# Optimization experiments

Hardware: AMD Instinct MI355X
Metric: run time of the kernel (lower is better)

Reference implementation:

```python
import jax, jax.numpy as jnp
import numpy as np

B, N, KD, VD, ID, H = 2, 2048, 1024, 1024, 1024, 16
HD = ID // H
SCALE = ID ** (-0.5)  # module quirk: scale uses inner_dim, not head_dim
EPS = 1e-5


def layernorm(x, g, b):
    mu = jnp.mean(x, axis=-1, keepdims=True)
    var = jnp.var(x, axis=-1, keepdims=True)
    return (x - mu) * jax.lax.rsqrt(var + EPS) * g + b


def setup_inputs() -> dict:
    key = jax.random.key(0)
    ks = jax.random.split(key, 12)
    d = {
        "keys": jax.random.normal(ks[0], (B, N, KD), jnp.float32),
        "values": jax.random.normal(ks[1], (B, N, VD), jnp.float32),
        "qk_norm_g": jnp.ones((KD,), jnp.float32),
        "qk_norm_b": jnp.zeros((KD,), jnp.float32),
        "value_norm_g": jnp.ones((VD,), jnp.float32),
        "value_norm_b": jnp.zeros((VD,), jnp.float32),
        "key_norm_g": jnp.ones((ID,), jnp.float32),
        "key_norm_b": jnp.zeros((ID,), jnp.float32),
        "query_norm_g": jnp.ones((ID,), jnp.float32),
        "query_norm_b": jnp.zeros((ID,), jnp.float32),
        "w_qk": jax.random.normal(ks[2], (KD, 2 * ID), jnp.float32) * (KD ** -0.5),
        "w_v": jax.random.normal(ks[3], (VD, ID), jnp.float32) * (VD ** -0.5),
        "w_out": jax.random.normal(ks[4], (ID, VD), jnp.float32) * (ID ** -0.5),
        "b_out": jnp.zeros((VD,), jnp.float32),
    }
    return d


def reference(keys, values, qk_norm_g, qk_norm_b, value_norm_g, value_norm_b,
              key_norm_g, key_norm_b, query_norm_g, query_norm_b,
              w_qk, w_v, w_out, b_out):
    keys = layernorm(keys, qk_norm_g, qk_norm_b)
    values = layernorm(values, value_norm_g, value_norm_b)
    qk = keys @ w_qk  # [B,N,2*ID]
    q, k = qk[..., :ID], qk[..., ID:]
    q = layernorm(q, query_norm_g, query_norm_b)
    k = layernorm(k, key_norm_g, key_norm_b)
    # b n (h d) -> b h n d
    q = q.reshape(B, N, H, HD).transpose(0, 2, 1, 3)
    k = k.reshape(B, N, H, HD).transpose(0, 2, 1, 3)
    v = (values @ w_v).reshape(B, N, H, HD).transpose(0, 2, 1, 3)
    dots = jnp.einsum('bhqd,bhkd->bhqk', q, k) * SCALE
    attn = jax.nn.softmax(dots, axis=-1)
    out = jnp.einsum('bhqk,bhkd->bhqd', attn, v)
    out = out.transpose(0, 2, 1, 3).reshape(B, N, ID)
    return out @ w_out + b_out
```

## Files before the change

### kernel.cpp

```cpp
#include <hip/hip_runtime.h>
#include <hip/hip_bf16.h>
#include <type_traits>


typedef __hip_bfloat16 bf16;
typedef __attribute__((ext_vector_type(8))) short bf16x8;
typedef __attribute__((ext_vector_type(4))) float f32x4;

#define MFMA_BF16(a, b, c) __builtin_amdgcn_mfma_f32_16x16x32_bf16((a), (b), (c), 0, 0, 0)

__device__ __forceinline__ float us2f(unsigned short u) {
  unsigned int v = ((unsigned int)u) << 16;
  return __builtin_bit_cast(float, v);
}

__device__ __forceinline__ unsigned pack_bf16x2(float a, float b) {
  union { __hip_bfloat162 h; unsigned u; } cv;
  cv.h = __float22bfloat162_rn(float2{a, b});
  return cv.u;
}

__device__ __forceinline__ unsigned pack_bf16x2_trunc(float a, float b) {
  return __builtin_amdgcn_perm(__builtin_bit_cast(unsigned, b),
                               __builtin_bit_cast(unsigned, a), 0x07060302u);
}

__device__ __forceinline__ void gl_lds16(const bf16* g, bf16* l) {
  __builtin_amdgcn_global_load_lds(
      (const __attribute__((address_space(1))) void*)g,
      (__attribute__((address_space(3))) void*)l, 16, 0, 0);
}

__device__ __forceinline__ void barrier_pinned() {
  __builtin_amdgcn_s_barrier();
  __builtin_amdgcn_sched_barrier(0);
}

template <typename TIN>
__device__ __forceinline__ void ln_core(
    const TIN* __restrict__ in, const float* __restrict__ gamma,
    const float* __restrict__ beta, bf16* __restrict__ out,
    int stride, int D, float sc, int row, float* red)
{
  const int t = threadIdx.x;
  float x0, x1, x2, x3;
  if constexpr (std::is_same_v<TIN, float>) {
    float4 u = *(const float4*)(in + (size_t)row * stride + t * 4);
    x0 = u.x; x1 = u.y; x2 = u.z; x3 = u.w;
  } else {
    ushort4 u = *(const ushort4*)(in + (size_t)row * stride + t * 4);
    x0 = us2f(u.x); x1 = us2f(u.y); x2 = us2f(u.z); x3 = us2f(u.w);
  }
  float s = x0 + x1 + x2 + x3;
  float s2 = x0 * x0 + x1 * x1 + x2 * x2 + x3 * x3;
#pragma unroll
  for (int m = 1; m < 64; m <<= 1) {
    s += __shfl_xor(s, m);
    s2 += __shfl_xor(s2, m);
  }
  const int w = t >> 6, lane = t & 63;
  if (lane == 0) { red[w] = s; red[4 + w] = s2; }
  __syncthreads();
  if (t == 0) {
    float S = red[0] + red[1] + red[2] + red[3];
    float S2 = red[4] + red[5] + red[6] + red[7];
    float mu = S / (float)D;
    float var = S2 / (float)D - mu * mu;
    red[8] = mu;
    red[9] = rsqrtf(var + 1e-5f);
  }
  __syncthreads();
  const float mu = red[8], rs = red[9];
  float4 g4 = *(const float4*)(gamma + t * 4);
  float4 b4 = *(const float4*)(beta + t * 4);
  uint2 o;
  o.x = pack_bf16x2(((x0 - mu) * rs * g4.x + b4.x) * sc, ((x1 - mu) * rs * g4.y + b4.y) * sc);
  o.y = pack_bf16x2(((x2 - mu) * rs * g4.z + b4.z) * sc, ((x3 - mu) * rs * g4.w + b4.w) * sc);
  *(uint2*)(out + (size_t)row * D + t * 4) = o;
}

template <typename TIN>
__global__ __launch_bounds__(256) void ln2_kernel(
    const TIN* __restrict__ in0, const TIN* __restrict__ in1, int stride,
    const float* __restrict__ g0, const float* __restrict__ b0,
    const float* __restrict__ g1, const float* __restrict__ b1,
    bf16* __restrict__ out0, bf16* __restrict__ out1, int D,
    float sc0, float sc1)
{
  __shared__ float red[10];
  const int which = blockIdx.y;
  ln_core<TIN>(which ? in1 : in0, which ? g1 : g0, which ? b1 : b0,
               which ? out1 : out0, stride, D, which ? sc1 : sc0,
               blockIdx.x, red);
}

__device__ __forceinline__ void transpose_core(
    const float* __restrict__ in, bf16* __restrict__ out, int C,
    int r0, int c0, float (*tile)[68])
{
  const int R = 1024;
  const int t = threadIdx.x;
  const int lr = t >> 2, lc = (t & 3) * 16;
  const float* src = in + (size_t)(r0 + lr) * C + (c0 + lc);
#pragma unroll
  for (int i = 0; i < 4; ++i) {
    float4 u = *(const float4*)(src + i * 4);
    tile[lr][lc + i * 4 + 0] = u.x;
    tile[lr][lc + i * 4 + 1] = u.y;
    tile[lr][lc + i * 4 + 2] = u.z;
    tile[lr][lc + i * 4 + 3] = u.w;
  }
  __syncthreads();
  __align__(16) bf16 tmp[16];
#pragma unroll
  for (int j = 0; j < 16; ++j) tmp[j] = __float2bfloat16(tile[lc + j][lr]);
  bf16* dst = out + (size_t)(c0 + lr) * R + (r0 + lc);
  *(bf16x8*)dst       = *(const bf16x8*)&tmp[0];
  *(bf16x8*)(dst + 8) = *(const bf16x8*)&tmp[8];
}

__global__ __launch_bounds__(256) void prep_kernel(
    const float* __restrict__ keys, const float* __restrict__ values,
    const float* __restrict__ qk_g, const float* __restrict__ qk_b,
    const float* __restrict__ val_g, const float* __restrict__ val_b,
    bf16* __restrict__ keys_ln, bf16* __restrict__ values_ln,
    const float* __restrict__ w_qk, bf16* __restrict__ wqkT,
    const float* __restrict__ w_v, bf16* __restrict__ wvT,
    const float* __restrict__ w_out, bf16* __restrict__ woutT)
{
  __shared__ float tile[64][68];
  __shared__ float red[10];
  const int bid = blockIdx.x;
  if (bid < 8192) {
    const int row = bid >> 1, which = bid & 1;
    ln_core<float>(which ? values : keys, which ? val_g : qk_g,
                   which ? val_b : qk_b, which ? values_ln : keys_ln,
                   1024, 1024, 1.0f, row, red);
  } else {
    const int tz = bid - 8192;
    if (tz < 512) {
      transpose_core(w_qk, wqkT, 2048, (tz >> 5) * 64, (tz & 31) * 64, tile);
    } else if (tz < 768) {
      const int s = tz - 512;
      transpose_core(w_v, wvT, 1024, (s >> 4) * 64, (s & 15) * 64, tile);
    } else {
      const int s = tz - 768;
      transpose_core(w_out, woutT, 1024, (s >> 4) * 64, (s & 15) * 64, tile);
    }
  }
}

template <int BM, int BN, int TMODE, typename TOUT>
__device__ __forceinline__ void gemm_core(
    const bf16* __restrict__ A, const bf16* __restrict__ Bt,
    const float* __restrict__ bias, TOUT* __restrict__ C,
    int N, int K, int has_bias, int bx, int by, bf16* smem)
{
  constexpr int MT = BM / 32, NT = BN / 32;
  constexpr int ASL = BM / 32, BSL = BN / 32;
  constexpr int BUFE = (BM + BN) * 64;
  const int t = threadIdx.x;
  const int w = t >> 6, lane = t & 63, l15 = lane & 15, quad = lane >> 4;
  const int wy = w >> 1, wx = w & 1;
  const bf16* Ab = A + (size_t)by * BM * K;
  const bf16* Bb = Bt + (size_t)bx * BN * K;
  f32x4 acc[MT][NT] = {};

  const bf16* aptr[ASL];
  const bf16* bptr[BSL];
#pragma unroll
  for (int i = 0; i < ASL; ++i) {
    int s = i * 256 + t, row = s >> 3, c = (s & 7) ^ (row & 7);
    aptr[i] = Ab + (size_t)row * K + (c << 3);
  }
#pragma unroll
  for (int i = 0; i < BSL; ++i) {
    int s = i * 256 + t, row = s >> 3, c = (s & 7) ^ (row & 7);
    bptr[i] = Bb + (size_t)row * K + (c << 3);
  }

  auto stage = [&](bf16* buf, int kc) {
#pragma unroll
    for (int i = 0; i < ASL; ++i)
      gl_lds16(aptr[i] + kc, buf + (i * 256 + t) * 8);
#pragma unroll
    for (int i = 0; i < BSL; ++i)
      gl_lds16(bptr[i] + kc, buf + BM * 64 + (i * 256 + t) * 8);
  };

  const int sw = (quad ^ (l15 & 7)) << 3;
  const int NK = K >> 6;

  stage(smem, 0);

  for (int kt = 0; kt < NK; ++kt) {
    const int cur = kt & 1;
    bf16* lA = smem + cur * BUFE;
    bf16* lB = lA + BM * 64;
    barrier_pinned();
    if (kt + 1 < NK) {
      stage(smem + (cur ^ 1) * BUFE, (kt + 1) << 6);
      if constexpr (ASL + BSL == 8)
        asm volatile("s_waitcnt vmcnt(8)" ::: "memory");
      else
        asm volatile("s_waitcnt vmcnt(6)" ::: "memory");
    } else {
      asm volatile("s_waitcnt vmcnt(0)" ::: "memory");
    }
    barrier_pinned();

#pragma unroll
    for (int h = 0; h < 2; ++h) {
      const int so = sw ^ (h << 5);
      bf16x8 af[MT], bfr[NT];
#pragma unroll
      for (int mt = 0; mt < MT; ++mt)
        af[mt] = *(const bf16x8*)&lA[(wy * (BM / 2) + mt * 16 + l15) * 64 + so];
#pragma unroll
      for (int nt = 0; nt < NT; ++nt)
        bfr[nt] = *(const bf16x8*)&lB[(wx * (BN / 2) + nt * 16 + l15) * 64 + so];
#pragma unroll
      for (int mt = 0; mt < MT; ++mt)
#pragma unroll
        for (int nt = 0; nt < NT; ++nt)
          acc[mt][nt] = MFMA_BF16(af[mt], bfr[nt], acc[mt][nt]);
    }
  }

  if constexpr (TMODE == 1) {
    constexpr int STR = BM + 8;
    static_assert(BN * STR <= 2 * BUFE, "lOut must fit staging buffers");
    bf16* lOut = smem;
    __syncthreads();
#pragma unroll
    for (int mt = 0; mt < MT; ++mt)
#pragma unroll
      for (int nt = 0; nt < NT; ++nt) {
        const int d = wx * (BN / 2) + nt * 16 + l15;
        const int n = wy * (BM / 2) + mt * 16 + quad * 4;
        uint2 pk;
        pk.x = pack_bf16x2(acc[mt][nt][0], acc[mt][nt][1]);
        pk.y = pack_bf16x2(acc[mt][nt][2], acc[mt][nt][3]);
        *(uint2*)&lOut[d * STR + n] = pk;
      }
    __syncthreads();
    const int row0 = by * BM;
    const int bidx = row0 >> 11, n0 = row0 & 2047;
    const int col0 = bx * BN;
    constexpr int CPR = BM / 32;
    constexpr int NITER = (BN * CPR) / 256;
#pragma unroll
    for (int it = 0; it < NITER; ++it) {
      const int idx = it * 256 + t;
      const int d = idx / CPR, off = (idx % CPR) * 32;
      const bf16* srcp = &lOut[d * STR + off];
      bf16* g = (bf16*)C + ((size_t)(bidx << 10) + col0 + d) * 2048 + n0 + off;
#pragma unroll
      for (int j = 0; j < 4; ++j)
        *(bf16x8*)(g + j * 8) = *(const bf16x8*)(srcp + j * 8);
    }
  } else {
    const int row_base = by * BM + wy * (BM / 2);
    const int col_base = bx * BN + wx * (BN / 2);
#pragma unroll
    for (int mt = 0; mt < MT; ++mt)
#pragma unroll
      for (int nt = 0; nt < NT; ++nt) {
        const int col = col_base + nt * 16 + l15;
        const float bb = has_bias ? bias[col] : 0.0f;
#pragma unroll
        for (int r = 0; r < 4; ++r) {
          const int row = row_base + mt * 16 + quad * 4 + r;
          float v = acc[mt][nt][r] + bb;
          if constexpr (std::is_same_v<TOUT, bf16>)
            C[(size_t)row * N + col] = __float2bfloat16(v);
          else
            C[(size_t)row * N + col] = v;
        }
      }
  }
}

template <int BM, int BN, int TMODE, typename TOUT>
__global__ __launch_bounds__(256) void gemm_bt_kernel(
    const bf16* __restrict__ A, const bf16* __restrict__ Bt,
    const float* __restrict__ bias, TOUT* __restrict__ C,
    int N, int K, int has_bias)
{
  __shared__ __align__(16) bf16 smem[2 * (BM + BN) * 64];
  gemm_core<BM, BN, TMODE, TOUT>(A, Bt, bias, C, N, K, has_bias,
                                 blockIdx.x, blockIdx.y, smem);
}

__global__ __launch_bounds__(256) void gemm_dual_kernel(
    const bf16* __restrict__ A0, const bf16* __restrict__ B0, bf16* __restrict__ C0,
    const bf16* __restrict__ A1, const bf16* __restrict__ B1, bf16* __restrict__ C1)
{
  __shared__ __align__(16) bf16 smem[2 * 256 * 64];
  const int bid = blockIdx.x;
  if (bid < 512) {
    gemm_core<128, 128, 0, bf16>(A0, B0, nullptr, C0, 2048, 1024, 0,
                                 bid & 15, bid >> 4, smem);
  } else {
    const int b = bid - 512;
    gemm_core<128, 128, 1, bf16>(A1, B1, nullptr, C1, 1024, 1024, 0,
                                 b & 7, b >> 3, smem);
  }
}

__global__ __launch_bounds__(256) void flash_kernel(
    const bf16* __restrict__ Q, const bf16* __restrict__ Km,
    const bf16* __restrict__ Vt, bf16* __restrict__ O)
{
  __shared__ __align__(16) bf16 smem[8192 + 8192 + 8192];
  bf16* lQ = smem;
  bf16* lKb = smem + 8192;
  bf16* lVb = smem + 16384;
  const int t = threadIdx.x;
  const int w = t >> 6, lane = t & 63, l15 = lane & 15, quad = lane >> 4;
  const int qt = blockIdx.x, bh = blockIdx.y;
  const int b = bh >> 4, h = bh & 15;
  const int qrow0 = b * 2048 + qt * 128;
  const bf16* qbase = Q + (size_t)qrow0 * 1024 + h * 64;
  const bf16* kbase = Km + ((size_t)(b * 2048)) * 1024 + h * 64;
  const bf16* vbase = Vt + ((size_t)(b * 1024 + h * 64)) * 2048;

  const int sr0 = t >> 3, sc0 = ((t & 7) ^ (sr0 & 7)) << 3;
  const int sr1 = (256 + t) >> 3, sc1 = (((256 + t) & 7) ^ (sr1 & 7)) << 3;
  const int gr0 = (sr0 & 0x23) | ((sr0 & 0x0C) << 1) | ((sr0 & 0x10) >> 2);
  const int gr1 = (sr1 & 0x23) | ((sr1 & 0x0C) << 1) | ((sr1 & 0x10) >> 2);
  const bf16* kp0 = kbase + gr0 * 1024 + sc0;
  const bf16* kp1 = kbase + gr1 * 1024 + sc1;
  const bf16* vp0 = vbase + sr0 * 2048 + sc0;
  const bf16* vp1 = vbase + sr1 * 2048 + sc1;

#pragma unroll
  for (int i = 0; i < 4; ++i) {
    int s = i * 256 + t;
    int row = s >> 3, c = (s & 7) ^ (row & 7);
    gl_lds16(qbase + (size_t)row * 1024 + (c << 3), lQ + s * 8);
  }
  gl_lds16(kp0, lKb + t * 8);
  gl_lds16(kp1, lKb + (256 + t) * 8);
  gl_lds16(vp0, lVb + t * 8);
  gl_lds16(vp1, lVb + (256 + t) * 8);
  asm volatile("s_waitcnt vmcnt(4)" ::: "memory");
  barrier_pinned();

  const int sw = (quad ^ (l15 & 7)) << 3;
  bf16x8 qf[2][2];
#pragma unroll
  for (int mset = 0; mset < 2; ++mset) {
    const int row = w * 32 + mset * 16 + l15;
    qf[mset][0] = *(const bf16x8*)&lQ[row * 64 + sw];
    qf[mset][1] = *(const bf16x8*)&lQ[row * 64 + (sw ^ 32)];
  }

  f32x4 o_acc[4][2] = {};
  f32x4 l_vec[2] = {};

  for (int kt = 0; kt < 32; ++kt) {
    const int cur = kt & 1;
    bf16* lK = lKb + cur * 4096;
    bf16* lV = lVb + cur * 4096;
    bf16* lKn = lKb + (cur ^ 1) * 4096;
    bf16* lVn = lVb + (cur ^ 1) * 4096;

    barrier_pinned();
    {
      const int ktn = (kt + 1) & 31;
      const int ko = ktn << 16;
      const int vo = ktn << 6;
      gl_lds16(kp0 + ko, lKn + t * 8);
      gl_lds16(kp1 + ko, lKn + (256 + t) * 8);
      gl_lds16(vp0 + vo, lVn + t * 8);
      gl_lds16(vp1 + vo, lVn + (256 + t) * 8);
    }
    asm volatile("s_waitcnt vmcnt(4)" ::: "memory");
    barrier_pinned();

    bf16x8 kf[4][2];
#pragma unroll
    for (int nt = 0; nt < 4; ++nt) {
      kf[nt][0] = *(const bf16x8*)&lK[(nt * 16 + l15) * 64 + sw];
      kf[nt][1] = *(const bf16x8*)&lK[(nt * 16 + l15) * 64 + (sw ^ 32)];
    }

    bf16x8 pa[2][2];
#pragma unroll
    for (int mset = 0; mset < 2; ++mset) {
#pragma unroll
      for (int half = 0; half < 2; ++half) {
        f32x4 z0 = {}, z1 = {};
        z0 = MFMA_BF16(kf[2 * half + 0][0], qf[mset][0], z0);
        z0 = MFMA_BF16(kf[2 * half + 0][1], qf[mset][1], z0);
        z1 = MFMA_BF16(kf[2 * half + 1][0], qf[mset][0], z1);
        z1 = MFMA_BF16(kf[2 * half + 1][1], qf[mset][1], z1);
        f32x4 p0, p1;
#pragma unroll
        for (int r = 0; r < 4; ++r) {
          p0[r] = __builtin_amdgcn_exp2f(z0[r]);
          p1[r] = __builtin_amdgcn_exp2f(z1[r]);
        }
        l_vec[mset] += p0 + p1;
        union { unsigned u[4]; bf16x8 v; } cv;
        cv.u[0] = pack_bf16x2_trunc(p0[0], p0[1]);
        cv.u[1] = pack_bf16x2_trunc(p0[2], p0[3]);
        cv.u[2] = pack_bf16x2_trunc(p1[0], p1[1]);
        cv.u[3] = pack_bf16x2_trunc(p1[2], p1[3]);
        pa[mset][half] = cv.v;
      }
    }

    bf16x8 vf[4][2];
#pragma unroll
    for (int dt = 0; dt < 4; ++dt) {
      vf[dt][0] = *(const bf16x8*)&lV[(dt * 16 + l15) * 64 + sw];
      vf[dt][1] = *(const bf16x8*)&lV[(dt * 16 + l15) * 64 + (sw ^ 32)];
    }

    __builtin_amdgcn_s_setprio(1);
#pragma unroll
    for (int mset = 0; mset < 2; ++mset)
#pragma unroll
      for (int dt = 0; dt < 4; ++dt) {
        o_acc[dt][mset] = MFMA_BF16(vf[dt][0], pa[mset][0], o_acc[dt][mset]);
        o_acc[dt][mset] = MFMA_BF16(vf[dt][1], pa[mset][1], o_acc[dt][mset]);
      }
    __builtin_amdgcn_s_setprio(0);
  }

#pragma unroll
  for (int mset = 0; mset < 2; ++mset) {
    float tsum = l_vec[mset][0] + l_vec[mset][1] + l_vec[mset][2] + l_vec[mset][3];
    tsum += __shfl_xor(tsum, 16);
    tsum += __shfl_xor(tsum, 32);
    const float inv = 1.0f / tsum;
    const int m = qrow0 + w * 32 + mset * 16 + l15;
#pragma unroll
    for (int dt = 0; dt < 4; ++dt) {
      uint2 ok;
      ok.x = pack_bf16x2(o_acc[dt][mset][0] * inv, o_acc[dt][mset][1] * inv);
      ok.y = pack_bf16x2(o_acc[dt][mset][2] * inv, o_acc[dt][mset][3] * inv);
      *(uint2*)&O[(size_t)m * 1024 + h * 64 + dt * 16 + quad * 4] = ok;
    }
  }
}

extern "C" void kernel_launch(void* const* d_in, const int* in_sizes, int n_in,
                              void* d_out, int out_size, void* d_ws, size_t ws_size,
                              hipStream_t stream)
{
  (void)in_sizes; (void)n_in; (void)out_size; (void)ws_size;
  const float* keys   = (const float*)d_in[0];
  const float* values = (const float*)d_in[1];
  const float* qk_g   = (const float*)d_in[2];
  const float* qk_b   = (const float*)d_in[3];
  const float* val_g  = (const float*)d_in[4];
  const float* val_b  = (const float*)d_in[5];
  const float* key_g  = (const float*)d_in[6];
  const float* key_b  = (const float*)d_in[7];
  const float* qry_g  = (const float*)d_in[8];
  const float* qry_b  = (const float*)d_in[9];
  const float* w_qk   = (const float*)d_in[10];
  const float* w_v    = (const float*)d_in[11];
  const float* w_out  = (const float*)d_in[12];
  const float* b_out  = (const float*)d_in[13];
  float* out = (float*)d_out;

  const float CEXP = 0.03125f * 1.44269504f;

  char* ws = (char*)d_ws;
  const size_t MB = 1024 * 1024;
  bf16* keys_ln   = (bf16*)(ws + 0);
  bf16* values_ln = (bf16*)(ws + 8 * MB);
  bf16* qk        = (bf16*)(ws + 16 * MB);
  bf16* vt        = (bf16*)(ws + 32 * MB);
  bf16* qln       = (bf16*)(ws + 0);
  bf16* kln       = (bf16*)(ws + 8 * MB);
  bf16* attn      = (bf16*)(ws + 16 * MB);
  bf16* wqkT      = (bf16*)(ws + 40 * MB);
  bf16* wvT       = (bf16*)(ws + 44 * MB);
  bf16* woutT     = (bf16*)(ws + 46 * MB);

  prep_kernel<<<dim3(9216), 256, 0, stream>>>(
      keys, values, qk_g, qk_b, val_g, val_b, keys_ln, values_ln,
      w_qk, wqkT, w_v, wvT, w_out, woutT);
  gemm_dual_kernel<<<dim3(768), 256, 0, stream>>>(
      keys_ln, wqkT, qk, values_ln, wvT, vt);
  ln2_kernel<bf16><<<dim3(4096, 2), 256, 0, stream>>>(
      qk, qk + 1024, 2048, qry_g, qry_b, key_g, key_b, qln, kln, 1024, CEXP, 1.0f);
  flash_kernel<<<dim3(16, 32), 256, 0, stream>>>(qln, kln, vt, attn);
  gemm_bt_kernel<128, 64, 0, float><<<dim3(16, 32), 256, 0, stream>>>(attn, woutT, b_out, out, 1024, 1024, 1);
}
```

Measured before the change: 219.5 us.

## Halve GEMM and flash tile sizes, add XCD-aware block swizzle, MFMA row sums

```diff
diff --git a/kernel.cpp b/kernel.cpp
--- a/kernel.cpp
+++ b/kernel.cpp
@@ -34,6 +34,10 @@
 __device__ __forceinline__ void barrier_pinned() {
   __builtin_amdgcn_s_barrier();
   __builtin_amdgcn_sched_barrier(0);
+}
+
+__device__ __forceinline__ int xcd_swz(int orig, int nwg) {
+  return (orig & 7) * (nwg >> 3) + (orig >> 3);
 }
 
 template <typename TIN>
@@ -288,23 +292,27 @@
     int N, int K, int has_bias)
 {
   __shared__ __align__(16) bf16 smem[2 * (BM + BN) * 64];
+  const int nwg = gridDim.x * gridDim.y;
+  const int orig = blockIdx.y * gridDim.x + blockIdx.x;
+  const int s = xcd_swz(orig, nwg);
   gemm_core<BM, BN, TMODE, TOUT>(A, Bt, bias, C, N, K, has_bias,
-                                 blockIdx.x, blockIdx.y, smem);
+                                 s % gridDim.x, s / gridDim.x, smem);
 }
 
 __global__ __launch_bounds__(256) void gemm_dual_kernel(
     const bf16* __restrict__ A0, const bf16* __restrict__ B0, bf16* __restrict__ C0,
     const bf16* __restrict__ A1, const bf16* __restrict__ B1, bf16* __restrict__ C1)
 {
-  __shared__ __align__(16) bf16 smem[2 * 256 * 64];
+  __shared__ __align__(16) bf16 smem[2 * 192 * 64];
   const int bid = blockIdx.x;
-  if (bid < 512) {
-    gemm_core<128, 128, 0, bf16>(A0, B0, nullptr, C0, 2048, 1024, 0,
-                                 bid & 15, bid >> 4, smem);
+  if (bid < 1024) {
+    const int s = xcd_swz(bid, 1024);
+    gemm_core<128, 64, 0, bf16>(A0, B0, nullptr, C0, 2048, 1024, 0,
+                                s & 31, s >> 5, smem);
   } else {
-    const int b = bid - 512;
-    gemm_core<128, 128, 1, bf16>(A1, B1, nullptr, C1, 1024, 1024, 0,
-                                 b & 7, b >> 3, smem);
+    const int s = xcd_swz(bid - 1024, 512);
+    gemm_core<128, 64, 1, bf16>(A1, B1, nullptr, C1, 1024, 1024, 0,
+                                s & 15, s >> 4, smem);
   }
 }
 
@@ -312,15 +320,17 @@
     const bf16* __restrict__ Q, const bf16* __restrict__ Km,
     const bf16* __restrict__ Vt, bf16* __restrict__ O)
 {
-  __shared__ __align__(16) bf16 smem[8192 + 8192 + 8192];
+  __shared__ __align__(16) bf16 smem[4096 + 8192 + 8192];
   bf16* lQ = smem;
-  bf16* lKb = smem + 8192;
-  bf16* lVb = smem + 16384;
+  bf16* lKb = smem + 4096;
+  bf16* lVb = smem + 4096 + 8192;
   const int t = threadIdx.x;
   const int w = t >> 6, lane = t & 63, l15 = lane & 15, quad = lane >> 4;
-  const int qt = blockIdx.x, bh = blockIdx.y;
+  const int bid = blockIdx.x;
+  const int qt = (bid >> 3) & 31;
+  const int bh = (bid & 7) + ((bid >> 8) << 3);
   const int b = bh >> 4, h = bh & 15;
-  const int qrow0 = b * 2048 + qt * 128;
+  const int qrow0 = b * 2048 + qt * 64;
   const bf16* qbase = Q + (size_t)qrow0 * 1024 + h * 64;
   const bf16* kbase = Km + ((size_t)(b * 2048)) * 1024 + h * 64;
   const bf16* vbase = Vt + ((size_t)(b * 1024 + h * 64)) * 2048;
@@ -335,7 +345,7 @@
   const bf16* vp1 = vbase + sr1 * 2048 + sc1;
 
 #pragma unroll
-  for (int i = 0; i < 4; ++i) {
+  for (int i = 0; i < 2; ++i) {
     int s = i * 256 + t;
     int row = s >> 3, c = (s & 7) ^ (row & 7);
     gl_lds16(qbase + (size_t)row * 1024 + (c << 3), lQ + s * 8);
@@ -348,16 +358,17 @@
   barrier_pinned();
 
   const int sw = (quad ^ (l15 & 7)) << 3;
-  bf16x8 qf[2][2];
-#pragma unroll
-  for (int mset = 0; mset < 2; ++mset) {
-    const int row = w * 32 + mset * 16 + l15;
-    qf[mset][0] = *(const bf16x8*)&lQ[row * 64 + sw];
-    qf[mset][1] = *(const bf16x8*)&lQ[row * 64 + (sw ^ 32)];
-  }
-
-  f32x4 o_acc[4][2] = {};
-  f32x4 l_vec[2] = {};
+  bf16x8 qf[2];
+  {
+    const int row = w * 16 + l15;
+    qf[0] = *(const bf16x8*)&lQ[row * 64 + sw];
+    qf[1] = *(const bf16x8*)&lQ[row * 64 + (sw ^ 32)];
+  }
+
+  f32x4 o_acc[4] = {};
+  f32x4 s_acc = {};
+  const short ONEB = (short)0x3F80;
+  const bf16x8 ones = {ONEB, ONEB, ONEB, ONEB, ONEB, ONEB, ONEB, ONEB};
 
   for (int kt = 0; kt < 32; ++kt) {
     const int cur = kt & 1;
@@ -386,30 +397,26 @@
       kf[nt][1] = *(const bf16x8*)&lK[(nt * 16 + l15) * 64 + (sw ^ 32)];
     }
 
-    bf16x8 pa[2][2];
-#pragma unroll
-    for (int mset = 0; mset < 2; ++mset) {
-#pragma unroll
-      for (int half = 0; half < 2; ++half) {
-        f32x4 z0 = {}, z1 = {};
-        z0 = MFMA_BF16(kf[2 * half + 0][0], qf[mset][0], z0);
-        z0 = MFMA_BF16(kf[2 * half + 0][1], qf[mset][1], z0);
-        z1 = MFMA_BF16(kf[2 * half + 1][0], qf[mset][0], z1);
-        z1 = MFMA_BF16(kf[2 * half + 1][1], qf[mset][1], z1);
-        f32x4 p0, p1;
-#pragma unroll
-        for (int r = 0; r < 4; ++r) {
-          p0[r] = __builtin_amdgcn_exp2f(z0[r]);
-          p1[r] = __builtin_amdgcn_exp2f(z1[r]);
-        }
-        l_vec[mset] += p0 + p1;
-        union { unsigned u[4]; bf16x8 v; } cv;
-        cv.u[0] = pack_bf16x2_trunc(p0[0], p0[1]);
-        cv.u[1] = pack_bf16x2_trunc(p0[2], p0[3]);
-        cv.u[2] = pack_bf16x2_trunc(p1[0], p1[1]);
-        cv.u[3] = pack_bf16x2_trunc(p1[2], p1[3]);
-        pa[mset][half] = cv.v;
+    bf16x8 pa[2];
+#pragma unroll
+    for (int half = 0; half < 2; ++half) {
+      f32x4 z0 = {}, z1 = {};
+      z0 = MFMA_BF16(kf[2 * half + 0][0], qf[0], z0);
+      z0 = MFMA_BF16(kf[2 * half + 0][1], qf[1], z0);
+      z1 = MFMA_BF16(kf[2 * half + 1][0], qf[0], z1);
+      z1 = MFMA_BF16(kf[2 * half + 1][1], qf[1], z1);
+      f32x4 p0, p1;
+#pragma unroll
+      for (int r = 0; r < 4; ++r) {
+        p0[r] = __builtin_amdgcn_exp2f(z0[r]);
+        p1[r] = __builtin_amdgcn_exp2f(z1[r]);
       }
+      union { unsigned u[4]; bf16x8 v; } cv;
+      cv.u[0] = pack_bf16x2_trunc(p0[0], p0[1]);
+      cv.u[1] = pack_bf16x2_trunc(p0[2], p0[3]);
+      cv.u[2] = pack_bf16x2_trunc(p1[0], p1[1]);
+      cv.u[3] = pack_bf16x2_trunc(p1[2], p1[3]);
+      pa[half] = cv.v;
     }
 
     bf16x8 vf[4][2];
@@ -420,28 +427,24 @@
     }
 
     __builtin_amdgcn_s_setprio(1);
-#pragma unroll
-    for (int mset = 0; mset < 2; ++mset)
-#pragma unroll
-      for (int dt = 0; dt < 4; ++dt) {
-        o_acc[dt][mset] = MFMA_BF16(vf[dt][0], pa[mset][0], o_acc[dt][mset]);
-        o_acc[dt][mset] = MFMA_BF16(vf[dt][1], pa[mset][1], o_acc[dt][mset]);
-      }
+    s_acc = MFMA_BF16(ones, pa[0], s_acc);
+    s_acc = MFMA_BF16(ones, pa[1], s_acc);
+#pragma unroll
+    for (int dt = 0; dt < 4; ++dt) {
+      o_acc[dt] = MFMA_BF16(vf[dt][0], pa[0], o_acc[dt]);
+      o_acc[dt] = MFMA_BF16(vf[dt][1], pa[1], o_acc[dt]);
+    }
     __builtin_amdgcn_s_setprio(0);
   }
 
-#pragma unroll
-  for (int mset = 0; mset < 2; ++mset) {
-    float tsum = l_vec[mset][0] + l_vec[mset][1] + l_vec[mset][2] + l_vec[mset][3];
-    tsum += __shfl_xor(tsum, 16);
-    tsum += __shfl_xor(tsum, 32);
-    const float inv = 1.0f / tsum;
-    const int m = qrow0 + w * 32 + mset * 16 + l15;
+  {
+    const float inv = 1.0f / s_acc[0];
+    const int m = qrow0 + w * 16 + l15;
 #pragma unroll
     for (int dt = 0; dt < 4; ++dt) {
       uint2 ok;
-      ok.x = pack_bf16x2(o_acc[dt][mset][0] * inv, o_acc[dt][mset][1] * inv);
-      ok.y = pack_bf16x2(o_acc[dt][mset][2] * inv, o_acc[dt][mset][3] * inv);
+      ok.x = pack_bf16x2(o_acc[dt][0] * inv, o_acc[dt][1] * inv);
+      ok.y = pack_bf16x2(o_acc[dt][2] * inv, o_acc[dt][3] * inv);
       *(uint2*)&O[(size_t)m * 1024 + h * 64 + dt * 16 + quad * 4] = ok;
     }
   }
@@ -486,10 +489,10 @@
   prep_kernel<<<dim3(9216), 256, 0, stream>>>(
       keys, values, qk_g, qk_b, val_g, val_b, keys_ln, values_ln,
       w_qk, wqkT, w_v, wvT, w_out, woutT);
-  gemm_dual_kernel<<<dim3(768), 256, 0, stream>>>(
+  gemm_dual_kernel<<<dim3(1536), 256, 0, stream>>>(
       keys_ln, wqkT, qk, values_ln, wvT, vt);
   ln2_kernel<bf16><<<dim3(4096, 2), 256, 0, stream>>>(
       qk, qk + 1024, 2048, qry_g, qry_b, key_g, key_b, qln, kln, 1024, CEXP, 1.0f);
-  flash_kernel<<<dim3(16, 32), 256, 0, stream>>>(qln, kln, vt, attn);
+  flash_kernel<<<dim3(1024), 256, 0, stream>>>(qln, kln, vt, attn);
   gemm_bt_kernel<128, 64, 0, float><<<dim3(16, 32), 256, 0, stream>>>(attn, woutT, b_out, out, 1024, 1024, 1);
 }
```

Result: no change. 222.9 us (+1.5%).
